# Performance work log

Hardware: AMD Instinct MI355X
Metric: run time of the kernel (lower is better)

The kernel has to match this reference:

```python
import jax, jax.numpy as jnp
import numpy as np

B, S, D, H = 16, 1024, 768, 12
HD = D // H
SCALE = HD ** -0.5


def setup_inputs() -> dict:
    key = jax.random.key(0)
    k1, k2, k3, k4 = jax.random.split(key, 4)
    # Xavier-uniform-like init for the linear weights
    lim_qkv = (6.0 / (D + 3 * D)) ** 0.5
    lim_proj = (6.0 / (D + D)) ** 0.5
    return {
        "hidden_states": jax.random.normal(k1, (B, S, D), dtype=jnp.float32),
        "mask": jax.random.randint(k2, (B, S), 0, 2).astype(bool),
        "qkv_w": jax.random.uniform(k3, (3 * D, D), minval=-lim_qkv, maxval=lim_qkv, dtype=jnp.float32),
        "qkv_b": jnp.zeros((3 * D,), dtype=jnp.float32),
        "proj_w": jax.random.uniform(k4, (D, D), minval=-lim_proj, maxval=lim_proj, dtype=jnp.float32),
        "proj_b": jnp.zeros((D,), dtype=jnp.float32),
    }


def _masked_softmax(scores, attn_mask):
    # scores: [B,H,S,S]; attn_mask: [B,1,S,S] bool. Fully-masked rows -> all-zero
    # weights (torch gives NaN there but then zeroes the output rows; zeroing
    # the weights yields the identical final output without NaNs).
    neg_inf = jnp.finfo(scores.dtype).min
    m = jnp.max(jnp.where(attn_mask, scores, neg_inf), axis=-1, keepdims=True)
    e = jnp.where(attn_mask, jnp.exp(scores - m), 0.0)
    denom = jnp.sum(e, axis=-1, keepdims=True)
    return e / jnp.where(denom == 0, 1.0, denom)


def reference(hidden_states, mask, qkv_w, qkv_b, proj_w, proj_b):
    # fused QKV projection: [B,S,3D]
    qkv = hidden_states @ qkv_w.T + qkv_b
    qkv = qkv.reshape(B, S, 3, H, HD).transpose(2, 0, 3, 1, 4)  # [3,B,H,S,hd]
    q, k, v = qkv[0], qkv[1], qkv[2]
    tok_mask = mask[:, None, :, None]  # [B,1,S,1]
    q = jnp.where(tok_mask, q, 0.0)
    k = jnp.where(tok_mask, k, 0.0)
    v = jnp.where(tok_mask, v, 0.0)
    scores = jnp.einsum("bhqd,bhkd->bhqk", q, k) * SCALE
    attn_mask = (mask[:, :, None] & mask[:, None, :])[:, None]  # [B,1,S,S]
    attn = _masked_softmax(scores, attn_mask)
    context = jnp.einsum("bhqk,bhkd->bhqd", attn, v)
    context = context.transpose(0, 2, 1, 3).reshape(B, S, D)
    out = context @ proj_w.T + proj_b
    out = jnp.where(mask[:, :, None], out, 0.0)
    return out
```

## Files before the change

### kernel.cpp

```cpp
#include <hip/hip_runtime.h>
#include <cstdint>
#include <cstddef>

#define B 16
#define S 1024
#define D 768
#define H 12
#define HD 64
#define NTOK (B * S)
#define QKV_N (3 * D)
#define SCALE 0.125f
#define C2 2.88539008f
#define GK 768
#define NT_K 12

typedef _Float16 f16x8 __attribute__((ext_vector_type(8)));
typedef _Float16 f16x4 __attribute__((ext_vector_type(4)));
typedef __fp16 fp16x2 __attribute__((ext_vector_type(2)));
typedef float f32x4 __attribute__((ext_vector_type(4)));
typedef int i32x4 __attribute__((ext_vector_type(4)));

typedef __attribute__((address_space(3))) void as3_void;
typedef const __attribute__((address_space(1))) void as1_void;

#if defined(__has_builtin)
#if __has_builtin(__builtin_amdgcn_exp2f)
#define EXP2(x) __builtin_amdgcn_exp2f(x)
#else
#define EXP2(x) exp2f(x)
#endif
#else
#define EXP2(x) exp2f(x)
#endif

#define BARRIER() asm volatile("s_barrier" ::: "memory")

union PPack { f16x8 h; i32x4 i; };
union CPack { fp16x2 h; int i; };

__global__ __launch_bounds__(256) void normalize_mask_kernel(
    const unsigned char* __restrict__ raw, int* __restrict__ outm, int n) {
    __shared__ int s_isbyte;
    const int tid = threadIdx.x;
    if (tid == 0) s_isbyte = 0;
    __syncthreads();
    int found = 0;
    for (int i = tid; i < n; i += 256) {
        if ((i & 3) != 0 && raw[i] != 0) found = 1;
    }
    if (found) atomicOr(&s_isbyte, 1);
    __syncthreads();
    const int isbyte = s_isbyte;
    if (isbyte) {
        for (int i = tid; i < n; i += 256) outm[i] = raw[i] ? 1 : 0;
    } else {
        const int* r32 = (const int*)raw;
        for (int i = tid; i < n; i += 256) outm[i] = r32[i] ? 1 : 0;
    }
}

__global__ __launch_bounds__(256) void cvt_all_f16(
    const float* __restrict__ in0, _Float16* __restrict__ out0, int n0,
    const float* __restrict__ in1, _Float16* __restrict__ out1, int n1,
    const float* __restrict__ in2, _Float16* __restrict__ out2, int n2) {
    int i = blockIdx.x * 256 + threadIdx.x;
    const float* in;
    _Float16* out;
    if (i < n0) { in = in0; out = out0; }
    else if (i < n0 + n1) { i -= n0; in = in1; out = out1; }
    else { i -= n0 + n1; in = in2; out = out2; if (i >= n2) return; }
    const float4 v = ((const float4*)in)[i];
    f16x4 o;
    o[0] = (_Float16)v.x; o[1] = (_Float16)v.y;
    o[2] = (_Float16)v.z; o[3] = (_Float16)v.w;
    ((f16x4*)out)[i] = o;
}

__global__ __launch_bounds__(512, 2) void gemm256(
    const _Float16* __restrict__ A, const _Float16* __restrict__ Wm,
    const float* __restrict__ bias, _Float16* __restrict__ outh,
    _Float16* __restrict__ vtb) {
    __shared__ _Float16 smem[65536];

    const int tid = threadIdx.x;
    const int w = tid >> 6, l = tid & 63;
    const int wr = w >> 2, wc = w & 3;
    const int wm = wr * 128, wn = wc * 64;
    const int lg = l >> 4, lc = l & 15;

    const int bid = blockIdx.x;
    const int xcd = bid & 7;
    const int idx = bid >> 3;
    const int bn = (idx >> 3) * 256;
    const int bm = (xcd * 8 + (idx & 7)) * 256;

    const int r0 = l >> 3;
    const int sw8 = ((l & 7) ^ (l >> 3)) * 8;

    f32x4 acc[8][4] = {};

#define STG(T, BUF)                                                            \
    {                                                                          \
        const int kt_ = (T) * 64;                                              \
        _Float16* sA_ = smem + (BUF) * 16384;                                  \
        _Float16* sB_ = smem + 32768 + (BUF) * 16384;                          \
        _Pragma("unroll")                                                      \
        for (int i_ = 0; i_ < 4; ++i_) {                                       \
            const int seg_ = i_ * 8 + w;                                       \
            const int rr_ = seg_ * 8 + r0;                                     \
            __builtin_amdgcn_global_load_lds(                                  \
                (as1_void*)(A + (size_t)(bm + rr_) * GK + kt_ + sw8),          \
                (as3_void*)(sA_ + seg_ * 512), 16, 0, 0);                      \
            __builtin_amdgcn_global_load_lds(                                  \
                (as1_void*)(Wm + (size_t)(bn + rr_) * GK + kt_ + sw8),         \
                (as3_void*)(sB_ + seg_ * 512), 16, 0, 0);                      \
        }                                                                      \
    }

    STG(0, 0)

    for (int t = 0; t < NT_K; ++t) {
        const int cur = t & 1;
        if (t + 1 < NT_K) {
            STG(t + 1, cur ^ 1)
            asm volatile("s_waitcnt vmcnt(8)" ::: "memory");
        } else {
            asm volatile("s_waitcnt vmcnt(0)" ::: "memory");
        }
        BARRIER();

        const _Float16* sA = smem + cur * 16384;
        const _Float16* sB = smem + 32768 + cur * 16384;
        __builtin_amdgcn_s_setprio(1);
#pragma unroll
        for (int kk = 0; kk < 2; ++kk) {
            const int c16 = ((kk << 2) + lg) ^ (lc & 7);
            f16x8 bf[4], af[8];
#pragma unroll
            for (int ni = 0; ni < 4; ++ni)
                bf[ni] = *(const f16x8*)&sB[(wn + ni * 16 + lc) * 64 + c16 * 8];
#pragma unroll
            for (int mi = 0; mi < 8; ++mi)
                af[mi] = *(const f16x8*)&sA[(wm + mi * 16 + lc) * 64 + c16 * 8];
#pragma unroll
            for (int mi = 0; mi < 8; ++mi)
#pragma unroll
                for (int ni = 0; ni < 4; ++ni)
                    acc[mi][ni] = __builtin_amdgcn_mfma_f32_16x16x32_f16(
                        af[mi], bf[ni], acc[mi][ni], 0, 0, 0);
        }
        __builtin_amdgcn_s_setprio(0);
        BARRIER();
    }
#undef STG

    float bs[4];
#pragma unroll
    for (int ni = 0; ni < 4; ++ni) bs[ni] = bias[bn + wn + ni * 16 + lc];

    if (bn < 1536) {
#pragma unroll
        for (int mi = 0; mi < 8; ++mi) {
#pragma unroll
            for (int j = 0; j < 4; ++j) {
                const int m = bm + wm + mi * 16 + lg * 4 + j;
#pragma unroll
                for (int ni = 0; ni < 4; ++ni) {
                    const int col = bn + wn + ni * 16 + lc;
                    outh[(size_t)m * QKV_N + col] =
                        (_Float16)(acc[mi][ni][j] + bs[ni]);
                }
            }
        }
    } else {
#pragma unroll
        for (int p = 0; p < 2; ++p) {
            BARRIER();
            if ((wc >> 1) == p) {
#pragma unroll
                for (int mi = 0; mi < 8; ++mi) {
#pragma unroll
                    for (int ni = 0; ni < 4; ++ni) {
                        f16x4 v4;
#pragma unroll
                        for (int j = 0; j < 4; ++j)
                            v4[j] = (_Float16)(acc[mi][ni][j] + bs[ni]);
                        const int cl = wn - p * 128 + ni * 16 + lc;
                        const int row = wm + mi * 16 + lg * 4;
                        *(f16x4*)&smem[cl * 264 + row] = v4;
                    }
                }
            }
            BARRIER();
            const int r = tid >> 2;
            const int c0 = (tid & 3) * 64;
            const int col0 = bn - 1536 + p * 128 + r;
            const int hh = col0 >> 6, hd = col0 & 63;
            const int bb = bm >> 10;
            const int s0 = (bm & 1023) + c0;
            _Float16* dst = vtb + ((size_t)(bb * H + hh) * HD + hd) * S + s0;
#pragma unroll
            for (int e = 0; e < 8; ++e)
                *(f16x8*)(dst + e * 8) = *(const f16x8*)&smem[r * 264 + c0 + e * 8];
        }
    }
}

__global__ __launch_bounds__(256, 2) void gemm_proj(
    const _Float16* __restrict__ A, const _Float16* __restrict__ Wm,
    const float* __restrict__ bias, const int* __restrict__ rowmask,
    float* __restrict__ outf) {
    __shared__ _Float16 smem[32768];

    const int tid = threadIdx.x;
    const int w = tid >> 6, l = tid & 63;
    const int wm = (w >> 1) * 64, wn = (w & 1) * 64;
    const int lg = l >> 4, lc = l & 15;

    const int bid = blockIdx.x;
    const int xcd = bid & 7;
    const int idx = bid >> 3;
    const int bn = (idx >> 4) * 128;
    const int bm = (xcd * 16 + (idx & 15)) * 128;

    f32x4 acc[4][4] = {};

#define STAGE(T, BUF)                                                           \
    {                                                                           \
        const int kt_ = (T) * 64;                                               \
        _Pragma("unroll")                                                       \
        for (int i_ = 0; i_ < 4; ++i_) {                                        \
            const int ci_ = (w << 2) + i_;                                      \
            const int r_ = (ci_ << 3) + (l >> 3);                               \
            const int c16_ = (l & 7) ^ (r_ & 7);                                \
            __builtin_amdgcn_global_load_lds(                                   \
                (as1_void*)(A + (size_t)(bm + r_) * GK + kt_ + c16_ * 8),       \
                (as3_void*)(smem + (BUF) * 8192 + ci_ * 512), 16, 0, 0);        \
            __builtin_amdgcn_global_load_lds(                                   \
                (as1_void*)(Wm + (size_t)(bn + r_) * GK + kt_ + c16_ * 8),      \
                (as3_void*)(smem + 16384 + (BUF) * 8192 + ci_ * 512), 16, 0, 0);\
        }                                                                       \
    }

    STAGE(0, 0)

    for (int t = 0; t < NT_K; ++t) {
        const int cur = t & 1;
        if (t + 1 < NT_K) {
            STAGE(t + 1, cur ^ 1)
            asm volatile("s_waitcnt vmcnt(8)" ::: "memory");
        } else {
            asm volatile("s_waitcnt vmcnt(0)" ::: "memory");
        }
        BARRIER();

        const _Float16* sA = smem + cur * 8192;
        const _Float16* sB = smem + 16384 + cur * 8192;
        __builtin_amdgcn_s_setprio(1);
#pragma unroll
        for (int kk = 0; kk < 2; ++kk) {
            const int c16 = ((kk << 2) + lg) ^ (lc & 7);
            f16x8 af[4], bf[4];
#pragma unroll
            for (int ni = 0; ni < 4; ++ni)
                bf[ni] = *(const f16x8*)&sB[(wn + ni * 16 + lc) * 64 + c16 * 8];
#pragma unroll
            for (int mi = 0; mi < 4; ++mi)
                af[mi] = *(const f16x8*)&sA[(wm + mi * 16 + lc) * 64 + c16 * 8];
#pragma unroll
            for (int mi = 0; mi < 4; ++mi)
#pragma unroll
                for (int ni = 0; ni < 4; ++ni)
                    acc[mi][ni] = __builtin_amdgcn_mfma_f32_16x16x32_f16(
                        af[mi], bf[ni], acc[mi][ni], 0, 0, 0);
        }
        __builtin_amdgcn_s_setprio(0);
        BARRIER();
    }
#undef STAGE

    float bs[4];
#pragma unroll
    for (int ni = 0; ni < 4; ++ni) bs[ni] = bias[bn + wn + ni * 16 + lc];

#pragma unroll
    for (int mi = 0; mi < 4; ++mi) {
#pragma unroll
        for (int j = 0; j < 4; ++j) {
            const int m = bm + wm + mi * 16 + lg * 4 + j;
            const int mv = rowmask[m];
#pragma unroll
            for (int ni = 0; ni < 4; ++ni) {
                const int col = bn + wn + ni * 16 + lc;
                outf[(size_t)m * D + col] = mv ? acc[mi][ni][j] + bs[ni] : 0.f;
            }
        }
    }
}

__global__ __launch_bounds__(256, 3) void attn_kernel(
    const _Float16* __restrict__ qkv, const _Float16* __restrict__ vtb,
    const int* __restrict__ mask, _Float16* __restrict__ ctx) {
    __shared__ _Float16 ksm[3][64 * 64];
    __shared__ _Float16 vsm[3][64 * 64];
    __shared__ float mbias[S];

    const int blk = blockIdx.x;
    const int xcd = blk & 7;
    const int idx = blk >> 3;
    const int bh_ = xcd * 24 + (idx >> 2);
    const int qt = idx & 3;
    const int h = bh_ % H;
    const int b = bh_ / H;
    const int tid = threadIdx.x;
    const int w = tid >> 6, lane = tid & 63;
    const int lg = lane >> 4, lc = lane & 15;

    const size_t bh = (size_t)(b * H + h);
    const _Float16* Kp = qkv + (size_t)(b * S) * QKV_N + D + h * HD;
    const _Float16* Vt = vtb + bh * HD * S;
    const int* mrow = mask + b * S;

    const int r0 = w * 8 + (lane >> 3);
    const int swz8 = ((lane & 7) ^ (r0 & 7)) * 8;
    const int koff0 = r0 * QKV_N + swz8;
    const int koff1 = (32 + r0) * QKV_N + swz8;
    const int voff0 = r0 * S + swz8;
    const int voff1 = (32 + r0) * S + swz8;

#define STAGE(T, BUF)                                                          \
    {                                                                          \
        const int kt_ = (T) * 64;                                              \
        __builtin_amdgcn_global_load_lds(                                      \
            (as1_void*)(Kp + (size_t)kt_ * QKV_N + koff0),                     \
            (as3_void*)(&ksm[BUF][w * 512]), 16, 0, 0);                        \
        __builtin_amdgcn_global_load_lds(                                      \
            (as1_void*)(Kp + (size_t)kt_ * QKV_N + koff1),                     \
            (as3_void*)(&ksm[BUF][2048 + w * 512]), 16, 0, 0);                 \
        __builtin_amdgcn_global_load_lds(                                      \
            (as1_void*)(Vt + (size_t)kt_ + voff0),                            \
            (as3_void*)(&vsm[BUF][w * 512]), 16, 0, 0);                        \
        __builtin_amdgcn_global_load_lds(                                      \
            (as1_void*)(Vt + (size_t)kt_ + voff1),                            \
            (as3_void*)(&vsm[BUF][2048 + w * 512]), 16, 0, 0);                 \
    }

    const int qbase = qt * 256 + w * 16 + lc;
    const _Float16 qs = (_Float16)(0.125f * 1.44269504f);
    f16x8 qf[4][2];
#pragma unroll
    for (int qg = 0; qg < 4; ++qg) {
        const _Float16* Qp =
            qkv + (size_t)(b * S + qbase + qg * 64) * QKV_N + h * HD;
        qf[qg][0] = *(const f16x8*)(Qp + lg * 8);
        qf[qg][1] = *(const f16x8*)(Qp + 32 + lg * 8);
        qf[qg][0] *= qs;
        qf[qg][1] *= qs;
    }

#pragma unroll
    for (int i = 0; i < 4; ++i)
        mbias[i * 256 + tid] = mrow[i * 256 + tid] ? -C2 : -1e9f;

    STAGE(0, 0)
    STAGE(1, 1)

    f32x4 acc[4][4] = {};
    float lsum[4] = {0.f, 0.f, 0.f, 0.f};
    fp16x2 ones;
    ones[0] = (__fp16)1.0f; ones[1] = (__fp16)1.0f;

    int cur = 0;
    for (int it = 0; it < S / 64; ++it) {
        if (it + 2 < S / 64) {
            int nb = cur + 2; if (nb >= 3) nb -= 3;
            STAGE(it + 2, nb)
        }
        if (it == 0)
            asm volatile("s_waitcnt vmcnt(8) lgkmcnt(0)" ::: "memory");
        else if (it + 2 < S / 64)
            asm volatile("s_waitcnt vmcnt(8)" ::: "memory");
        else if (it + 2 == S / 64)
            asm volatile("s_waitcnt vmcnt(4)" ::: "memory");
        else
            asm volatile("s_waitcnt vmcnt(0)" ::: "memory");
        BARRIER();

        __builtin_amdgcn_s_setprio(1);
#pragma unroll
        for (int u = 0; u < 2; ++u) {
            PPack pp8[4];
#pragma unroll
            for (int s = 0; s < 2; ++s) {
                const int t = 2 * u + s;
                const int krow = (t * 16 + lc) * 64;
                const f16x8 kfa =
                    *(const f16x8*)&ksm[cur][krow + (lg ^ (lc & 7)) * 8];
                const f16x8 kfb =
                    *(const f16x8*)&ksm[cur][krow + ((4 + lg) ^ (lc & 7)) * 8];
                const f32x4 mb = *(const f32x4*)&mbias[it * 64 + t * 16 + 4 * lg];
#pragma unroll
                for (int qg = 0; qg < 4; ++qg) {
                    f32x4 c = mb;
                    c = __builtin_amdgcn_mfma_f32_16x16x32_f16(kfa, qf[qg][0], c, 0, 0, 0);
                    c = __builtin_amdgcn_mfma_f32_16x16x32_f16(kfb, qf[qg][1], c, 0, 0, 0);
                    CPack u0, u1;
                    u0.h = __builtin_amdgcn_cvt_pkrtz(EXP2(c[0]), EXP2(c[1]));
                    u1.h = __builtin_amdgcn_cvt_pkrtz(EXP2(c[2]), EXP2(c[3]));
                    lsum[qg] = __builtin_amdgcn_fdot2(u0.h, ones, lsum[qg], false);
                    lsum[qg] = __builtin_amdgcn_fdot2(u1.h, ones, lsum[qg], false);
                    pp8[qg].i[s * 2 + 0] = u0.i;
                    pp8[qg].i[s * 2 + 1] = u1.i;
                }
            }

#pragma unroll
            for (int g = 0; g < 4; ++g) {
                const int vrow = (g * 16 + lc) * 64;
                const int cA = ((4 * u + (lg >> 1)) ^ (lc & 7)) * 8 + (lg & 1) * 4;
                const int cB = ((4 * u + 2 + (lg >> 1)) ^ (lc & 7)) * 8 + (lg & 1) * 4;
                const f16x4 vlo = *(const f16x4*)&vsm[cur][vrow + cA];
                const f16x4 vhi = *(const f16x4*)&vsm[cur][vrow + cB];
                f16x8 vf8;
                vf8[0] = vlo[0]; vf8[1] = vlo[1]; vf8[2] = vlo[2]; vf8[3] = vlo[3];
                vf8[4] = vhi[0]; vf8[5] = vhi[1]; vf8[6] = vhi[2]; vf8[7] = vhi[3];
#pragma unroll
                for (int qg = 0; qg < 4; ++qg)
                    acc[qg][g] = __builtin_amdgcn_mfma_f32_16x16x32_f16(
                        pp8[qg].h, vf8, acc[qg][g], 0, 0, 0);
            }
        }
        __builtin_amdgcn_s_setprio(0);
        BARRIER();
        if (++cur >= 3) cur = 0;
    }
#undef STAGE

#pragma unroll
    for (int qg = 0; qg < 4; ++qg) {
        float l = lsum[qg];
        l += __shfl_xor(l, 16);
        l += __shfl_xor(l, 32);
        const float inv = l > 0.f ? 1.f / l : 0.f;
#pragma unroll
        for (int j = 0; j < 4; ++j) {
            const int qin = 4 * lg + j;
            const float ij = __shfl(inv, qin);
            const int qr = qt * 256 + qg * 64 + w * 16 + qin;
            const float iq = mrow[qr] ? ij : 0.f;
            const size_t o = ((size_t)(b * S + qr)) * D + h * HD;
#pragma unroll
            for (int g = 0; g < 4; ++g)
                ctx[o + 16 * g + lc] = (_Float16)(acc[qg][g][j] * iq);
        }
    }
}

extern "C" void kernel_launch(void* const* d_in, const int* in_sizes, int n_in,
                              void* d_out, int out_size, void* d_ws, size_t ws_size,
                              hipStream_t stream) {
    const float* hidden = (const float*)d_in[0];
    const unsigned char* maskraw = (const unsigned char*)d_in[1];
    const float* qkv_w = (const float*)d_in[2];
    const float* qkv_b = (const float*)d_in[3];
    const float* proj_w = (const float*)d_in[4];
    const float* proj_b = (const float*)d_in[5];
    float* out = (float*)d_out;

    char* ws = (char*)d_ws;
    size_t off = 0;
    int* maskN = (int*)(ws + off);            off += (size_t)NTOK * 4;
    _Float16* hid16 = (_Float16*)(ws + off);  off += (size_t)NTOK * D * 2;
    _Float16* qkvw16 = (_Float16*)(ws + off); off += (size_t)QKV_N * D * 2;
    _Float16* projw16 = (_Float16*)(ws + off); off += (size_t)D * D * 2;
    _Float16* qkv16 = (_Float16*)(ws + off);  off += (size_t)NTOK * QKV_N * 2;
    _Float16* vt = (_Float16*)(ws + off);     off += (size_t)NTOK * D * 2;
    _Float16* ctx16 = (_Float16*)(ws + off);  off += (size_t)NTOK * D * 2;

    normalize_mask_kernel<<<1, 256, 0, stream>>>(maskraw, maskN, NTOK);

    const int n0 = NTOK * D / 4, n1 = QKV_N * D / 4, n2 = D * D / 4;
    cvt_all_f16<<<(n0 + n1 + n2 + 255) / 256, 256, 0, stream>>>(
        hidden, hid16, n0, qkv_w, qkvw16, n1, proj_w, projw16, n2);

    gemm256<<<dim3(576), 512, 0, stream>>>(hid16, qkvw16, qkv_b, qkv16, vt);

    attn_kernel<<<dim3(B * H * (S / 256)), 256, 0, stream>>>(qkv16, vt, maskN, ctx16);

    gemm_proj<<<dim3(768), 256, 0, stream>>>(ctx16, projw16, proj_b, maskN, out);
}
```

Measured before the change: 215.8 us.

## Interleave GEMM prefetch into K-loop phases and reorder attention staging barrier

The QKV GEMM main loop is split into four half-tile phases per K step. Each phase issues a quarter of the next tile's global-to-LDS loads between its fragment reads and MFMA blocks, so memory traffic is spread across the compute instead of issued in one burst. The attention loop now waits and synchronizes first, then issues the stage-ahead load, which drops the trailing barrier per iteration. This adds more barriers inside the GEMM loop, and the attention reorder relies on the triple buffer to stay race-free.

```diff
diff --git a/kernel.cpp b/kernel.cpp
--- a/kernel.cpp
+++ b/kernel.cpp
@@ -94,65 +94,87 @@
     const int bn = (idx >> 3) * 256;
     const int bm = (xcd * 8 + (idx & 7)) * 256;
 
-    const int r0 = l >> 3;
-    const int sw8 = ((l & 7) ^ (l >> 3)) * 8;
+    const int lrow = l >> 3;
+    const int sw8 = ((l & 7) ^ lrow) * 8;
 
     f32x4 acc[8][4] = {};
 
-#define STG(T, BUF)                                                            \
+#define STGH(GP, GB, LBASE, ROWB, KT, BUF)                                     \
     {                                                                          \
-        const int kt_ = (T) * 64;                                              \
-        _Float16* sA_ = smem + (BUF) * 16384;                                  \
-        _Float16* sB_ = smem + 32768 + (BUF) * 16384;                          \
         _Pragma("unroll")                                                      \
-        for (int i_ = 0; i_ < 4; ++i_) {                                       \
-            const int seg_ = i_ * 8 + w;                                       \
-            const int rr_ = seg_ * 8 + r0;                                     \
+        for (int i_ = 0; i_ < 2; ++i_) {                                       \
+            const int rb_ = (ROWB) + i_ * 64 + w * 8;                          \
             __builtin_amdgcn_global_load_lds(                                  \
-                (as1_void*)(A + (size_t)(bm + rr_) * GK + kt_ + sw8),          \
-                (as3_void*)(sA_ + seg_ * 512), 16, 0, 0);                      \
-            __builtin_amdgcn_global_load_lds(                                  \
-                (as1_void*)(Wm + (size_t)(bn + rr_) * GK + kt_ + sw8),         \
-                (as3_void*)(sB_ + seg_ * 512), 16, 0, 0);                      \
+                (as1_void*)((GP) + (size_t)((GB) + rb_ + lrow) * GK + (KT) + sw8), \
+                (as3_void*)(smem + (LBASE) + (BUF) * 16384 + rb_ * 64), 16, 0, 0); \
         }                                                                      \
     }
 
-    STG(0, 0)
+    STGH(A, bm, 0, 0, 0, 0)
+    STGH(A, bm, 0, 128, 0, 0)
+    STGH(Wm, bn, 32768, 0, 0, 0)
+    STGH(Wm, bn, 32768, 128, 0, 0)
+    asm volatile("s_waitcnt vmcnt(0)" ::: "memory");
+    BARRIER();
 
     for (int t = 0; t < NT_K; ++t) {
         const int cur = t & 1;
-        if (t + 1 < NT_K) {
-            STG(t + 1, cur ^ 1)
-            asm volatile("s_waitcnt vmcnt(8)" ::: "memory");
-        } else {
-            asm volatile("s_waitcnt vmcnt(0)" ::: "memory");
-        }
-        BARRIER();
-
+        const int nxt = cur ^ 1;
+        const int ktn = (t + 1) * 64;
+        const bool pf = (t + 1 < NT_K);
         const _Float16* sA = smem + cur * 16384;
         const _Float16* sB = smem + 32768 + cur * 16384;
-        __builtin_amdgcn_s_setprio(1);
+
 #pragma unroll
         for (int kk = 0; kk < 2; ++kk) {
             const int c16 = ((kk << 2) + lg) ^ (lc & 7);
-            f16x8 bf[4], af[8];
+            f16x8 bf[4], af[4];
+
 #pragma unroll
             for (int ni = 0; ni < 4; ++ni)
                 bf[ni] = *(const f16x8*)&sB[(wn + ni * 16 + lc) * 64 + c16 * 8];
 #pragma unroll
-            for (int mi = 0; mi < 8; ++mi)
-                af[mi] = *(const f16x8*)&sA[(wm + mi * 16 + lc) * 64 + c16 * 8];
-#pragma unroll
-            for (int mi = 0; mi < 8; ++mi)
+            for (int i = 0; i < 4; ++i)
+                af[i] = *(const f16x8*)&sA[(wm + i * 16 + lc) * 64 + c16 * 8];
+            if (pf) {
+                if (kk == 0) STGH(A, bm, 0, 0, ktn, nxt)
+                else         STGH(Wm, bn, 32768, 0, ktn, nxt)
+            }
+            BARRIER();
+            asm volatile("s_waitcnt lgkmcnt(0)" ::: "memory");
+            __builtin_amdgcn_s_setprio(1);
+#pragma unroll
+            for (int i = 0; i < 4; ++i)
 #pragma unroll
                 for (int ni = 0; ni < 4; ++ni)
-                    acc[mi][ni] = __builtin_amdgcn_mfma_f32_16x16x32_f16(
-                        af[mi], bf[ni], acc[mi][ni], 0, 0, 0);
-        }
-        __builtin_amdgcn_s_setprio(0);
-        BARRIER();
-    }
-#undef STG
+                    acc[i][ni] = __builtin_amdgcn_mfma_f32_16x16x32_f16(
+                        af[i], bf[ni], acc[i][ni], 0, 0, 0);
+            __builtin_amdgcn_s_setprio(0);
+            BARRIER();
+
+#pragma unroll
+            for (int i = 0; i < 4; ++i)
+                af[i] = *(const f16x8*)&sA[(wm + (4 + i) * 16 + lc) * 64 + c16 * 8];
+            if (pf) {
+                if (kk == 0) STGH(A, bm, 0, 128, ktn, nxt)
+                else         STGH(Wm, bn, 32768, 128, ktn, nxt)
+            }
+            BARRIER();
+            asm volatile("s_waitcnt lgkmcnt(0)" ::: "memory");
+            __builtin_amdgcn_s_setprio(1);
+#pragma unroll
+            for (int i = 0; i < 4; ++i)
+#pragma unroll
+                for (int ni = 0; ni < 4; ++ni)
+                    acc[4 + i][ni] = __builtin_amdgcn_mfma_f32_16x16x32_f16(
+                        af[i], bf[ni], acc[4 + i][ni], 0, 0, 0);
+            __builtin_amdgcn_s_setprio(0);
+            if (kk == 1 && pf)
+                asm volatile("s_waitcnt vmcnt(0)" ::: "memory");
+            BARRIER();
+        }
+    }
+#undef STGH
 
     float bs[4];
 #pragma unroll
@@ -372,19 +394,18 @@
 
     int cur = 0;
     for (int it = 0; it < S / 64; ++it) {
-        if (it + 2 < S / 64) {
-            int nb = cur + 2; if (nb >= 3) nb -= 3;
-            STAGE(it + 2, nb)
-        }
         if (it == 0)
-            asm volatile("s_waitcnt vmcnt(8) lgkmcnt(0)" ::: "memory");
-        else if (it + 2 < S / 64)
-            asm volatile("s_waitcnt vmcnt(8)" ::: "memory");
-        else if (it + 2 == S / 64)
+            asm volatile("s_waitcnt vmcnt(4) lgkmcnt(0)" ::: "memory");
+        else if (it < S / 64 - 1)
             asm volatile("s_waitcnt vmcnt(4)" ::: "memory");
         else
             asm volatile("s_waitcnt vmcnt(0)" ::: "memory");
         BARRIER();
+
+        if (it + 2 < S / 64) {
+            int nb = cur + 2; if (nb >= 3) nb -= 3;
+            STAGE(it + 2, nb)
+        }
 
         __builtin_amdgcn_s_setprio(1);
 #pragma unroll
@@ -431,7 +452,6 @@
             }
         }
         __builtin_amdgcn_s_setprio(0);
-        BARRIER();
         if (++cur >= 3) cur = 0;
     }
 #undef STAGE
```

After: 207.5 us. -3.8%, faster.
